# Kernel tuning notes

Hardware: AMD Instinct MI355X
Metric: run time of the kernel (lower is better)

The kernel has to match this reference:

```python
import jax, jax.numpy as jnp
import numpy as np

SCORE_THRESH = 0.05
NMS_THRESH = 0.5
K = 1000            # max NMS candidates (fixed for jit; padded/masked)
IMG_W, IMG_H = 1333, 800


def setup_inputs() -> dict:
    key = jax.random.key(0)
    k1, k2, k3 = jax.random.split(key, 3)
    N, C = 200000, 81
    class_logits = jax.random.normal(k1, (N, C), dtype=jnp.float32) * 2.0
    # well-formed xyxy boxes inside the image
    cxcy = jax.random.uniform(k2, (N, 2), dtype=jnp.float32) * jnp.array([IMG_W, IMG_H], jnp.float32)
    wh = jax.random.uniform(k3, (N, 2), dtype=jnp.float32) * 200.0 + 1.0
    boxes = jnp.concatenate([cxcy - wh * 0.5, cxcy + wh * 0.5], axis=-1)
    return {"class_logits": class_logits, "boxes": boxes}


def _pairwise_iou(b):
    # b: [K, 4] xyxy -> [K, K]
    area = (b[:, 2] - b[:, 0]) * (b[:, 3] - b[:, 1])
    lt = jnp.maximum(b[:, None, :2], b[None, :, :2])
    rb = jnp.minimum(b[:, None, 2:], b[None, :, 2:])
    wh = jnp.clip(rb - lt, 0.0)
    inter = wh[..., 0] * wh[..., 1]
    return inter / (area[:, None] + area[None, :] - inter + 1e-9)


def reference(class_logits, boxes):
    N, C = class_logits.shape
    prob = jax.nn.softmax(class_logits, axis=-1)            # [N, C]
    # clip_to_image (TO_REMOVE=1 convention: clamp to size-1)
    bx = jnp.stack([
        jnp.clip(boxes[:, 0], 0.0, IMG_W - 1),
        jnp.clip(boxes[:, 1], 0.0, IMG_H - 1),
        jnp.clip(boxes[:, 2], 0.0, IMG_W - 1),
        jnp.clip(boxes[:, 3], 0.0, IMG_H - 1),
    ], axis=-1)                                             # [N, 4]
    flat = prob.reshape(-1)                                 # [N*C], class = idx % C
    idx = jnp.arange(N * C)
    valid = (flat > SCORE_THRESH) & (idx % C != 0)          # fg + score threshold
    masked = jnp.where(valid, flat, -jnp.inf)
    top_scores, top_idx = jax.lax.top_k(masked, K)          # sorted descending
    prop_idx = top_idx // C
    cls = top_idx % C
    bk = bx[prop_idx]                                       # [K, 4]
    valid_k = jnp.isfinite(top_scores)
    scores_k = jnp.where(valid_k, top_scores, 0.0)
    # class-aware greedy NMS over the (sorted) top-K candidates
    conflict = (_pairwise_iou(bk) > NMS_THRESH) & (cls[:, None] == cls[None, :])
    rng = jnp.arange(K)

    def body(i, keep):
        sup = jnp.any(keep & conflict[:, i] & (rng < i))
        return keep.at[i].set(keep[i] & ~sup)

    keep = jax.lax.fori_loop(0, K, body, valid_k)
    out = jnp.concatenate([bk, scores_k[:, None]], axis=-1) * keep[:, None].astype(bk.dtype)
    return out  # [K, 5]: (x1, y1, x2, y2, score), zeroed where suppressed/invalid
```

## Files before the change

### kernel.cpp

```cpp
#include <hip/hip_runtime.h>
#include <stdint.h>
#include <math.h>

#define N_CLS    81
#define TOPK     1000
#define LISTCAP  (1u << 21)
#define CAP2     16384
#define SCORE_TH 0.05f
#define IMG_W    1333.0f
#define IMG_H    800.0f
#define GH_REP   8

#define GH_BASE  1905

#define OFF_CNT    0
#define OFF_CNT2   128
#define OFF_ARRV   256
#define OFF_TICKA  384
#define OFF_TICKR  640
#define OFF_TICKC  768
#define OFF_PBCA   896
#define OFF_TB     1024
#define OFF_GH     1280
#define OFF_RH     5376
#define MEMSET_BYTES 9472
#define OFF_SEL    16768
#define OFF_SEL2   16793984
#define OFF_BOX    16925056
#define OFF_SCORE  16941056
#define OFF_CLS    16945056
#define OFF_MASK   16949056

#define ROWS_PER_BLK 128
#define TILE_FLOATS  (ROWS_PER_BLK * N_CLS)
#define CBUF_CAP     1024
#define TAIL_BLOCKS  128
#define PADK         1016

typedef unsigned long long u64;

__device__ __forceinline__ int ipad(int j) { return j + (j >> 6); }

__device__ __forceinline__ void gload_lds16(const float* g, float* l) {
    __builtin_amdgcn_global_load_lds(
        (const __attribute__((address_space(1))) unsigned int*)g,
        (__attribute__((address_space(3))) unsigned int*)l, 16, 0, 0);
}

__device__ __forceinline__ unsigned agent_load_u32(const unsigned* p) {
    return __hip_atomic_load(p, __ATOMIC_RELAXED, __HIP_MEMORY_SCOPE_AGENT);
}
__device__ __forceinline__ u64 agent_load_u64(const u64* p) {
    return __hip_atomic_load(p, __ATOMIC_RELAXED, __HIP_MEMORY_SCOPE_AGENT);
}
__device__ __forceinline__ void agent_store_u32(unsigned* p, unsigned v) {
    __hip_atomic_store(p, v, __ATOMIC_RELAXED, __HIP_MEMORY_SCOPE_AGENT);
}
__device__ __forceinline__ void agent_store_u64(u64* p, u64 v) {
    __hip_atomic_store(p, v, __ATOMIC_RELAXED, __HIP_MEMORY_SCOPE_AGENT);
}
__device__ __forceinline__ void drain_vm() {
    asm volatile("s_waitcnt vmcnt(0)" ::: "memory");
}

__global__ __launch_bounds__(256) void k_pass1(
        const float* __restrict__ logits, int nrows,
        u64* __restrict__ sel, unsigned* __restrict__ cnt,
        unsigned* __restrict__ ghist) {
    __shared__ float tile[TILE_FLOATS];
    __shared__ unsigned lh[128];
    __shared__ u64 cbuf[CBUF_CAP];
    __shared__ unsigned lcnt, gbase;
    int tid = threadIdx.x, wv = tid >> 6, ln = tid & 63;
    for (int i = tid; i < 128; i += 256) lh[i] = 0;
    if (tid == 0) lcnt = 0;

    int base = blockIdx.x * ROWS_PER_BLK;
    int nr = nrows - base; if (nr > ROWS_PER_BLK) nr = ROWS_PER_BLK;
    const float* gtile = logits + (size_t)base * N_CLS;

    if (nr == ROWS_PER_BLK) {
        #pragma unroll
        for (int it = 0; it < 10; ++it) {
            int c = it * 1024 + wv * 256;
            gload_lds16(gtile + c + ln * 4, tile + c);
        }
        if (tid < TILE_FLOATS - 10240) tile[10240 + tid] = gtile[10240 + tid];
    } else {
        for (int i = tid; i < nr * N_CLS; i += 256) tile[i] = gtile[i];
    }
    __syncthreads();

    int r = tid >> 1, h = tid & 1;
    if (r < nr) {
        const int rb = r * N_CLS + h;
        float v[41];
        #pragma unroll
        for (int m = 0; m < 40; ++m) v[m] = tile[rb + 2 * m];
        v[40] = (h == 0) ? tile[rb + 80] : 0.0f;

        float mx = v[0];
        #pragma unroll
        for (int m = 1; m < 40; ++m) mx = fmaxf(mx, v[m]);
        mx = fmaxf(mx, (h == 0) ? v[40] : v[0]);
        float om = __shfl_xor(mx, 1);
        float mrow = fmaxf(mx, om);

        #pragma unroll
        for (int m = 0; m < 40; ++m) v[m] = expf(v[m] - mrow);
        v[40] = (h == 0) ? expf(v[40] - mrow) : 0.0f;

        float stk0 = 0.f, stk1 = 0.f, stk2 = 0.f, stk3 = 0.f, stk4 = 0.f;
        float S = 0.f;
        #pragma unroll
        for (int i = 0; i < 32; ++i) {
            const int b = ((i & 1) << 4) | ((i & 2) << 2) | (i & 4) |
                          ((i & 8) >> 2) | ((i & 16) >> 4);
            float x = v[b];
            if (b < 8) x += v[b + 32];
            else if (b == 8) x = (h == 0) ? x + v[40] : x;
            if (i & 1) { x = stk0 + x;
              if (i & 2) { x = stk1 + x;
                if (i & 4) { x = stk2 + x;
                  if (i & 8) { x = stk3 + x;
                    if (i & 16) { S = stk4 + x; } else stk4 = x;
                  } else stk3 = x;
                } else stk2 = x;
              } else stk1 = x;
            } else stk0 = x;
        }
        float oS = __shfl_xor(S, 1);
        float s = (h == 0) ? (S + oS) : (oS + S);

        float eth = 0.0499f * s;
        unsigned rowflat = (unsigned)(base + r) * N_CLS + (unsigned)h;
        #pragma unroll
        for (int m = 0; m < 41; ++m) {
            float e = v[m];
            if ((m + h) != 0 && e > eth) {
                float p = e / s;
                if (p > SCORE_TH) {
                    unsigned fb = __float_as_uint(p);
                    atomicAdd(&lh[(fb >> 19) - GH_BASE], 1u);
                    u64 key = ((u64)fb << 32) | (u64)(0xFFFFFFu - (rowflat + 2u * (unsigned)m));
                    unsigned pos = atomicAdd(&lcnt, 1u);
                    if (pos < CBUF_CAP) cbuf[pos] = key;
                    else { unsigned gp = atomicAdd(cnt, 1u); if (gp < LISTCAP) sel[gp] = key; }
                }
            }
        }
    }
    __syncthreads();
    unsigned* gh = ghist + (blockIdx.x & (GH_REP - 1)) * 128;
    for (int i = tid; i < 128; i += 256) {
        unsigned vv = lh[i];
        if (vv) atomicAdd(&gh[i], vv);
    }
    unsigned total = lcnt; if (total > CBUF_CAP) total = CBUF_CAP;
    if (tid == 0) gbase = atomicAdd(cnt, total);
    __syncthreads();
    unsigned gb = gbase;
    for (unsigned i = tid; i < total; i += 256) {
        unsigned gp = gb + i;
        if (gp < LISTCAP) sel[gp] = cbuf[i];
    }
}

__global__ __launch_bounds__(1024) void k_tail(
        char* __restrict__ ws, const float* __restrict__ boxes,
        float* __restrict__ out) {
    unsigned* cnt   = (unsigned*)(ws + OFF_CNT);
    unsigned* cnt2  = (unsigned*)(ws + OFF_CNT2);
    unsigned* arrv  = (unsigned*)(ws + OFF_ARRV);
    unsigned* tickA = (unsigned*)(ws + OFF_TICKA);
    unsigned* tickR = (unsigned*)(ws + OFF_TICKR);
    unsigned* tickC = (unsigned*)(ws + OFF_TICKC);
    u64*      pbca  = (u64*)(ws + OFF_PBCA);
    unsigned* ptb   = (unsigned*)(ws + OFF_TB);
    unsigned* ghist = (unsigned*)(ws + OFF_GH);
    unsigned* rhist = (unsigned*)(ws + OFF_RH);
    u64*      sel   = (u64*)(ws + OFF_SEL);
    u64*      sel2  = (u64*)(ws + OFF_SEL2);
    u64*      boxB  = (u64*)(ws + OFF_BOX);
    unsigned* scrB  = (unsigned*)(ws + OFF_SCORE);
    unsigned* clsB  = (unsigned*)(ws + OFF_CLS);
    u64*      mask  = (u64*)(ws + OFF_MASK);

    __shared__ unsigned scu[1024], sfu[1024];
    __shared__ union {
        unsigned lhist[1024];
        struct {
            float x1[PADK], y1[PADK], x2[PADK], y2[PADK];
            int cls[PADK]; unsigned sc[PADK];
        } c;
    } shu;
    __shared__ u64 words[16];
    __shared__ int schanged, swB;
    __shared__ unsigned swCA, sarr, stk, sfl, stb;
    __shared__ u64 spb;

    int tid = threadIdx.x, ln = tid & 63;
    unsigned nb = gridDim.x;

    if (tid == 0) sarr = atomicAdd(arrv, 1u);
    __syncthreads();
    if (sarr == 0) {
        if (tid < 128) {
            unsigned c = 0;
            #pragma unroll
            for (int rr = 0; rr < GH_REP; ++rr) c += ghist[rr * 128 + tid];
            scu[tid] = c; sfu[tid] = c;
        }
        if (tid == 0) swB = -1;
        __syncthreads();
        #pragma unroll
        for (int off = 1; off < 128; off <<= 1) {
            unsigned a = 0;
            if (tid < 128) a = (tid + off < 128) ? sfu[tid + off] : 0u;
            __syncthreads();
            if (tid < 128) sfu[tid] += a;
            __syncthreads();
        }
        if (tid == 0) swCA = sfu[0];
        __syncthreads();
        if (tid < 128) {
            unsigned incl = sfu[tid], excl = incl - scu[tid];
            if (excl < TOPK && incl >= TOPK) { swB = tid; swCA = excl; }
        }
        __syncthreads();
        if (tid == 0) {
            u64 pk = (1ull << 63) | ((u64)(swCA & 0x3FFu) << 8) | (u64)(unsigned)(swB + 1);
            agent_store_u64(pbca, pk);
        }
    }
    if (tid == 0) {
        u64 v;
        do { __builtin_amdgcn_s_sleep(2); v = agent_load_u64(pbca); } while (!(v >> 63));
        spb = v;
    }
    __syncthreads();
    int B = (int)(unsigned)(spb & 0xFFull) - 1;
    unsigned CA = (unsigned)((spb >> 8) & 0x3FFu);
    unsigned M = *cnt; if (M > LISTCAP) M = LISTCAP;
    unsigned stride = nb * 1024u;
    unsigned tbc = (B < 0) ? 0u : ((unsigned)(B + GH_BASE) << 19);
    unsigned Bbits = (unsigned)(B + GH_BASE);

    shu.lhist[tid] = 0;
    __syncthreads();
    for (unsigned ibase = blockIdx.x * 1024u; ibase < M; ibase += stride) {
        unsigned i = ibase + tid;
        bool act = (i < M);
        u64 key = act ? sel[i] : 0ull;
        unsigned bv = (unsigned)(key >> 32);
        if (act && B >= 0 && (bv >> 19) == Bbits)
            atomicAdd(&shu.lhist[(bv >> 9) & 1023u], 1u);
        bool c = act && (bv >= tbc) && (B >= 0 || true) && (key != 0ull);
        u64 b = __ballot(c);
        int n = __popcll(b);
        if (n) {
            unsigned wb = 0;
            if (ln == 0) wb = atomicAdd(cnt2, (unsigned)n);
            wb = __shfl(wb, 0);
            if (c) {
                unsigned pos = wb + (unsigned)__popcll(b & ((1ull << ln) - 1ull));
                if (pos < CAP2) agent_store_u64(&sel2[pos], key);
            }
        }
    }
    __syncthreads();
    { unsigned vv = shu.lhist[tid]; if (vv) atomicAdd(&rhist[tid], vv); }
    __syncthreads();
    drain_vm();
    if (tid == 0) stk = atomicAdd(tickA, 1u);
    __syncthreads();
    if (stk == nb - 1) {
        unsigned c = agent_load_u32(&rhist[tid]);
        scu[tid] = c; sfu[tid] = c;
        if (tid == 0) stb = 0;
        __syncthreads();
        #pragma unroll
        for (int off = 1; off < 1024; off <<= 1) {
            unsigned a = (tid + off < 1024) ? sfu[tid + off] : 0u;
            __syncthreads();
            sfu[tid] += a;
            __syncthreads();
        }
        unsigned incl = sfu[tid], excl = incl - scu[tid];
        if (B >= 0 && CA + excl < TOPK && CA + incl >= TOPK)
            stb = ((unsigned)(B + GH_BASE) << 19) | ((unsigned)tid << 9);
        __syncthreads();
        if (tid == 0) agent_store_u32(ptb, stb | 0x80000000u);
    }
    if (tid == 0) {
        unsigned f;
        do { __builtin_amdgcn_s_sleep(2); f = agent_load_u32(ptb); } while (!(f >> 31));
        sfl = f;
    }
    __syncthreads();
    unsigned tb = sfl & 0x7FFFFFFFu;

    {
        unsigned S = agent_load_u32(cnt2); if (S > CAP2) S = CAP2;
        unsigned slot = blockIdx.x * 16u + (unsigned)(tid >> 6);
        unsigned nslots = nb * 16u;
        unsigned lim = (S > TOPK) ? S : TOPK;
        for (unsigned k = slot; k < lim; k += nslots) {
            if (k < S) {
                u64 my = agent_load_u64(&sel2[k]);
                if ((unsigned)(my >> 32) < tb) continue;
                unsigned rk = 0;
                for (unsigned j = ln; j < S; j += 64)
                    rk += (agent_load_u64(&sel2[j]) > my) ? 1u : 0u;
                #pragma unroll
                for (int off = 32; off > 0; off >>= 1) rk += __shfl_xor(rk, off);
                if (ln == 0 && rk < TOPK) {
                    float sc = __uint_as_float((unsigned)(my >> 32));
                    unsigned fi = 0xFFFFFFu - (unsigned)(my & 0xFFFFFFFFull);
                    unsigned prop = fi / N_CLS;
                    int cls = (int)(fi - prop * N_CLS);
                    const float* bx = boxes + (size_t)prop * 4;
                    float x1 = fminf(fmaxf(bx[0], 0.0f), IMG_W - 1.0f);
                    float y1 = fminf(fmaxf(bx[1], 0.0f), IMG_H - 1.0f);
                    float x2 = fminf(fmaxf(bx[2], 0.0f), IMG_W - 1.0f);
                    float y2 = fminf(fmaxf(bx[3], 0.0f), IMG_H - 1.0f);
                    agent_store_u64(&boxB[rk * 2],
                        ((u64)__float_as_uint(y1) << 32) | __float_as_uint(x1));
                    agent_store_u64(&boxB[rk * 2 + 1],
                        ((u64)__float_as_uint(y2) << 32) | __float_as_uint(x2));
                    agent_store_u32(&scrB[rk], __float_as_uint(sc));
                    agent_store_u32(&clsB[rk], (unsigned)cls);
                }
            } else if (ln == 0) {
                agent_store_u64(&boxB[k * 2], 0ull);
                agent_store_u64(&boxB[k * 2 + 1], 0ull);
                agent_store_u32(&scrB[k], 0u);
                agent_store_u32(&clsB[k], (unsigned)-1);
            }
        }
    }
    __syncthreads();
    drain_vm();
    if (tid == 0) stk = atomicAdd(tickR, 1u);
    __syncthreads();
    if (blockIdx.x >= 16) return;
    if (tid == 0) {
        unsigned v;
        do { __builtin_amdgcn_s_sleep(2); v = agent_load_u32(tickR); } while (v < nb);
    }
    __syncthreads();

    if (tid < TOPK) {
        u64 a = agent_load_u64(&boxB[tid * 2]);
        u64 b = agent_load_u64(&boxB[tid * 2 + 1]);
        int ip = ipad(tid);
        shu.c.x1[ip] = __uint_as_float((unsigned)a);
        shu.c.y1[ip] = __uint_as_float((unsigned)(a >> 32));
        shu.c.x2[ip] = __uint_as_float((unsigned)b);
        shu.c.y2[ip] = __uint_as_float((unsigned)(b >> 32));
        shu.c.cls[ip] = (int)agent_load_u32(&clsB[tid]);
        shu.c.sc[ip]  = agent_load_u32(&scrB[tid]);
    }
    __syncthreads();
    {
        int t = blockIdx.x * 1024 + tid;
        int i = t >> 4, w = t & 15;
        if (i < TOPK) {
            int ip = ipad(i);
            float x1 = shu.c.x1[ip], y1 = shu.c.y1[ip];
            float x2 = shu.c.x2[ip], y2 = shu.c.y2[ip];
            int ci = shu.c.cls[ip];
            float ai = (x2 - x1) * (y2 - y1);
            u64 m = 0;
            int jbase = w << 6;
            for (int jj = 0; jj < 64; jj++) {
                int j = jbase + jj;
                if (j >= TOPK) break;
                int jp = ipad(j);
                float u1 = shu.c.x1[jp], w1 = shu.c.y1[jp];
                float u2 = shu.c.x2[jp], w2 = shu.c.y2[jp];
                float aj = (u2 - u1) * (w2 - w1);
                float ww = fmaxf(fminf(x2, u2) - fmaxf(x1, u1), 0.0f);
                float hh = fmaxf(fminf(y2, w2) - fmaxf(y1, w1), 0.0f);
                float inter = ww * hh;
                float iou = inter / (ai + aj - inter + 1e-9f);
                if (iou > 0.5f && ci == shu.c.cls[jp]) m |= (1ull << jj);
            }
            agent_store_u64(&mask[(size_t)i * 16 + w], m);
        }
    }
    __syncthreads();
    drain_vm();
    if (tid == 0) stk = atomicAdd(tickC, 1u);
    __syncthreads();
    if (stk != 15u) return;

    int wv = tid >> 6;
    int myip = ipad(tid < TOPK ? tid : 0);
    bool valid = (tid < TOPK) && (__uint_as_float(shu.c.sc[myip]) > 0.0f);
    u64 row[16];
    #pragma unroll
    for (int w = 0; w < 16; w++)
        row[w] = (tid < TOPK) ? agent_load_u64(&mask[(size_t)tid * 16 + w]) : 0ull;
    u64 lowmask = (1ull << ln) - 1ull;
    bool keep = valid;
    for (int it = 0; it < 1024; ++it) {
        u64 b = __ballot(keep);
        if (ln == 0) words[wv] = b;
        if (tid == 0) schanged = 0;
        __syncthreads();
        u64 sup = 0;
        for (int w = 0; w <= wv; w++) {
            u64 kw = words[w];
            if (w == wv) kw &= lowmask;
            sup |= row[w] & kw;
        }
        bool nk = valid && (sup == 0ull);
        if (nk != keep) schanged = 1;
        keep = nk;
        __syncthreads();
        if (!schanged) break;
    }
    if (tid < TOPK) {
        float sc = __uint_as_float(shu.c.sc[myip]);
        out[tid * 5 + 0] = keep ? shu.c.x1[myip] : 0.0f;
        out[tid * 5 + 1] = keep ? shu.c.y1[myip] : 0.0f;
        out[tid * 5 + 2] = keep ? shu.c.x2[myip] : 0.0f;
        out[tid * 5 + 3] = keep ? shu.c.y2[myip] : 0.0f;
        out[tid * 5 + 4] = keep ? sc : 0.0f;
    }
}

extern "C" void kernel_launch(void* const* d_in, const int* in_sizes, int n_in,
                              void* d_out, int out_size, void* d_ws, size_t ws_size,
                              hipStream_t stream) {
    const float* logits = (const float*)d_in[0];
    const float* boxes  = (const float*)d_in[1];
    float* out = (float*)d_out;
    int nrows = in_sizes[0] / N_CLS;

    char* w = (char*)d_ws;
    unsigned* cnt   = (unsigned*)(w + OFF_CNT);
    unsigned* ghist = (unsigned*)(w + OFF_GH);
    u64* sel        = (u64*)(w + OFF_SEL);

    hipMemsetAsync(w, 0, MEMSET_BYTES, stream);

    int nblk = (nrows + ROWS_PER_BLK - 1) / ROWS_PER_BLK;
    k_pass1<<<nblk, 256, 0, stream>>>(logits, nrows, sel, cnt, ghist);
    k_tail<<<TAIL_BLOCKS, 1024, 0, stream>>>(w, boxes, out);
}
```

Before: 186.1 us.

## Compute thresholds redundantly per block and cut tail grid to fewer blocks

Each tail block now computes the coarse histogram prefix scan itself instead of one elected block publishing it through a flag that the others spin on. After a global arrival barrier, every block also redundantly scans the refined histogram to get the exact threshold. Stream compaction into sel2 now issues one atomic per block iteration instead of one per wave, at the cost of extra block barriers. The tail grid shrinks from 128 to 32 blocks, which lowers spin-barrier cost and redundant work but leaves less parallelism for the filtering and ranking loops.

```diff
diff --git a/kernel.cpp b/kernel.cpp
--- a/kernel.cpp
+++ b/kernel.cpp
@@ -15,12 +15,9 @@
 
 #define OFF_CNT    0
 #define OFF_CNT2   128
-#define OFF_ARRV   256
 #define OFF_TICKA  384
 #define OFF_TICKR  640
 #define OFF_TICKC  768
-#define OFF_PBCA   896
-#define OFF_TB     1024
 #define OFF_GH     1280
 #define OFF_RH     5376
 #define MEMSET_BYTES 9472
@@ -34,7 +31,7 @@
 #define ROWS_PER_BLK 128
 #define TILE_FLOATS  (ROWS_PER_BLK * N_CLS)
 #define CBUF_CAP     1024
-#define TAIL_BLOCKS  128
+#define TAIL_BLOCKS  32
 #define PADK         1016
 
 typedef unsigned long long u64;
@@ -171,12 +168,9 @@
         float* __restrict__ out) {
     unsigned* cnt   = (unsigned*)(ws + OFF_CNT);
     unsigned* cnt2  = (unsigned*)(ws + OFF_CNT2);
-    unsigned* arrv  = (unsigned*)(ws + OFF_ARRV);
     unsigned* tickA = (unsigned*)(ws + OFF_TICKA);
     unsigned* tickR = (unsigned*)(ws + OFF_TICKR);
     unsigned* tickC = (unsigned*)(ws + OFF_TICKC);
-    u64*      pbca  = (u64*)(ws + OFF_PBCA);
-    unsigned* ptb   = (unsigned*)(ws + OFF_TB);
     unsigned* ghist = (unsigned*)(ws + OFF_GH);
     unsigned* rhist = (unsigned*)(ws + OFF_RH);
     u64*      sel   = (u64*)(ws + OFF_SEL);
@@ -195,52 +189,39 @@
         } c;
     } shu;
     __shared__ u64 words[16];
+    __shared__ unsigned wcnt[16], wpre[16];
     __shared__ int schanged, swB;
-    __shared__ unsigned swCA, sarr, stk, sfl, stb;
-    __shared__ u64 spb;
+    __shared__ unsigned swCA, stk, stb, sbase;
 
     int tid = threadIdx.x, ln = tid & 63;
+    int wv16 = tid >> 6;
     unsigned nb = gridDim.x;
 
-    if (tid == 0) sarr = atomicAdd(arrv, 1u);
-    __syncthreads();
-    if (sarr == 0) {
-        if (tid < 128) {
-            unsigned c = 0;
-            #pragma unroll
-            for (int rr = 0; rr < GH_REP; ++rr) c += ghist[rr * 128 + tid];
-            scu[tid] = c; sfu[tid] = c;
-        }
-        if (tid == 0) swB = -1;
-        __syncthreads();
-        #pragma unroll
-        for (int off = 1; off < 128; off <<= 1) {
-            unsigned a = 0;
-            if (tid < 128) a = (tid + off < 128) ? sfu[tid + off] : 0u;
-            __syncthreads();
-            if (tid < 128) sfu[tid] += a;
-            __syncthreads();
-        }
-        if (tid == 0) swCA = sfu[0];
-        __syncthreads();
-        if (tid < 128) {
-            unsigned incl = sfu[tid], excl = incl - scu[tid];
-            if (excl < TOPK && incl >= TOPK) { swB = tid; swCA = excl; }
-        }
-        __syncthreads();
-        if (tid == 0) {
-            u64 pk = (1ull << 63) | ((u64)(swCA & 0x3FFu) << 8) | (u64)(unsigned)(swB + 1);
-            agent_store_u64(pbca, pk);
-        }
-    }
-    if (tid == 0) {
-        u64 v;
-        do { __builtin_amdgcn_s_sleep(2); v = agent_load_u64(pbca); } while (!(v >> 63));
-        spb = v;
-    }
-    __syncthreads();
-    int B = (int)(unsigned)(spb & 0xFFull) - 1;
-    unsigned CA = (unsigned)((spb >> 8) & 0x3FFu);
+    if (tid < 128) {
+        unsigned c = 0;
+        #pragma unroll
+        for (int rr = 0; rr < GH_REP; ++rr) c += ghist[rr * 128 + tid];
+        scu[tid] = c; sfu[tid] = c;
+    }
+    if (tid == 0) swB = -1;
+    __syncthreads();
+    #pragma unroll
+    for (int off = 1; off < 128; off <<= 1) {
+        unsigned a = 0;
+        if (tid < 128) a = (tid + off < 128) ? sfu[tid + off] : 0u;
+        __syncthreads();
+        if (tid < 128) sfu[tid] += a;
+        __syncthreads();
+    }
+    if (tid == 0) swCA = sfu[0];
+    __syncthreads();
+    if (tid < 128) {
+        unsigned incl = sfu[tid], excl = incl - scu[tid];
+        if (excl < TOPK && incl >= TOPK) { swB = tid; swCA = excl; }
+    }
+    __syncthreads();
+    int B = swB;
+    unsigned CA = swCA;
     unsigned M = *cnt; if (M > LISTCAP) M = LISTCAP;
     unsigned stride = nb * 1024u;
     unsigned tbc = (B < 0) ? 0u : ((unsigned)(B + GH_BASE) << 19);
@@ -255,27 +236,37 @@
         unsigned bv = (unsigned)(key >> 32);
         if (act && B >= 0 && (bv >> 19) == Bbits)
             atomicAdd(&shu.lhist[(bv >> 9) & 1023u], 1u);
-        bool c = act && (bv >= tbc) && (B >= 0 || true) && (key != 0ull);
+        bool c = act && (bv >= tbc) && (key != 0ull);
         u64 b = __ballot(c);
         int n = __popcll(b);
-        if (n) {
-            unsigned wb = 0;
-            if (ln == 0) wb = atomicAdd(cnt2, (unsigned)n);
-            wb = __shfl(wb, 0);
-            if (c) {
-                unsigned pos = wb + (unsigned)__popcll(b & ((1ull << ln) - 1ull));
-                if (pos < CAP2) agent_store_u64(&sel2[pos], key);
-            }
+        if (ln == 0) wcnt[wv16] = (unsigned)n;
+        __syncthreads();
+        if (tid == 0) {
+            unsigned tot = 0;
+            #pragma unroll
+            for (int w = 0; w < 16; ++w) { wpre[w] = tot; tot += wcnt[w]; }
+            sbase = tot ? atomicAdd(cnt2, tot) : 0u;
+        }
+        __syncthreads();
+        if (c) {
+            unsigned pos = sbase + wpre[wv16] + (unsigned)__popcll(b & ((1ull << ln) - 1ull));
+            if (pos < CAP2) agent_store_u64(&sel2[pos], key);
         }
     }
     __syncthreads();
     { unsigned vv = shu.lhist[tid]; if (vv) atomicAdd(&rhist[tid], vv); }
     __syncthreads();
     drain_vm();
-    if (tid == 0) stk = atomicAdd(tickA, 1u);
-    __syncthreads();
-    if (stk == nb - 1) {
-        unsigned c = agent_load_u32(&rhist[tid]);
+    if (tid == 0) {
+        atomicAdd(tickA, 1u);
+        unsigned v;
+        do { __builtin_amdgcn_s_sleep(2); v = agent_load_u32(tickA); } while (v < nb);
+    }
+    __syncthreads();
+
+    unsigned tb = 0;
+    {
+        unsigned c = (B >= 0) ? agent_load_u32(&rhist[tid]) : 0u;
         scu[tid] = c; sfu[tid] = c;
         if (tid == 0) stb = 0;
         __syncthreads();
@@ -290,19 +281,12 @@
         if (B >= 0 && CA + excl < TOPK && CA + incl >= TOPK)
             stb = ((unsigned)(B + GH_BASE) << 19) | ((unsigned)tid << 9);
         __syncthreads();
-        if (tid == 0) agent_store_u32(ptb, stb | 0x80000000u);
-    }
-    if (tid == 0) {
-        unsigned f;
-        do { __builtin_amdgcn_s_sleep(2); f = agent_load_u32(ptb); } while (!(f >> 31));
-        sfl = f;
-    }
-    __syncthreads();
-    unsigned tb = sfl & 0x7FFFFFFFu;
+        tb = stb;
+    }
 
     {
         unsigned S = agent_load_u32(cnt2); if (S > CAP2) S = CAP2;
-        unsigned slot = blockIdx.x * 16u + (unsigned)(tid >> 6);
+        unsigned slot = blockIdx.x * 16u + (unsigned)wv16;
         unsigned nslots = nb * 16u;
         unsigned lim = (S > TOPK) ? S : TOPK;
         for (unsigned k = slot; k < lim; k += nslots) {
@@ -395,7 +379,7 @@
     __syncthreads();
     if (stk != 15u) return;
 
-    int wv = tid >> 6;
+    int wvv = tid >> 6;
     int myip = ipad(tid < TOPK ? tid : 0);
     bool valid = (tid < TOPK) && (__uint_as_float(shu.c.sc[myip]) > 0.0f);
     u64 row[16];
@@ -406,13 +390,13 @@
     bool keep = valid;
     for (int it = 0; it < 1024; ++it) {
         u64 b = __ballot(keep);
-        if (ln == 0) words[wv] = b;
+        if (ln == 0) words[wvv] = b;
         if (tid == 0) schanged = 0;
         __syncthreads();
         u64 sup = 0;
-        for (int w = 0; w <= wv; w++) {
+        for (int w = 0; w <= wvv; w++) {
             u64 kw = words[w];
-            if (w == wv) kw &= lowmask;
+            if (w == wvv) kw &= lowmask;
             sup |= row[w] & kw;
         }
         bool nk = valid && (sup == 0ull);
```

Result: slower. 202.2 us (+8.6%).
